# Performance work log

Hardware: AMD Instinct MI355X
Metric: run time of the kernel (lower is better)

Reference implementation:

```python
import jax, jax.numpy as jnp
import numpy as np

EMB_DIM = 1024
HEAD_DIM = 128
BLOCK_SIZE = 2048
BATCH = 8


def setup_inputs() -> dict:
    key = jax.random.key(0)
    kx, kq, kk, kv = jax.random.split(key, 4)
    x = jax.random.normal(kx, (BATCH, BLOCK_SIZE, EMB_DIM), dtype=jnp.float32)
    # nn.Linear(emb_dim, head_dim, bias=False) weights have shape [head_dim, emb_dim]
    s = 1.0 / np.sqrt(EMB_DIM)
    Wq = jax.random.uniform(kq, (HEAD_DIM, EMB_DIM), jnp.float32, -s, s)
    Wk = jax.random.uniform(kk, (HEAD_DIM, EMB_DIM), jnp.float32, -s, s)
    Wv = jax.random.uniform(kv, (HEAD_DIM, EMB_DIM), jnp.float32, -s, s)
    return {"x": x, "Wq": Wq, "Wk": Wk, "Wv": Wv}


def reference(x, Wq, Wk, Wv):
    # x: [b, t, c]; W*: [h, c]  (torch Linear applies x @ W.T)
    b, t, c = x.shape
    h = Wq.shape[0]
    q = jnp.einsum("btc,hc->bth", x, Wq)
    k = jnp.einsum("btc,hc->bth", x, Wk)
    v = jnp.einsum("btc,hc->bth", x, Wv)
    scores = jnp.einsum("bth,bsh->bts", q, k) * (h ** -0.5)  # [b, t, t]
    causal = jnp.tril(jnp.ones((t, t), dtype=bool))
    scores = jnp.where(causal, scores, -jnp.inf)
    attn = jax.nn.softmax(scores, axis=-1)
    # dropout is identity in eval / deterministic mode
    return jnp.einsum("bts,bsh->bth", attn, v)
```

## Files before the change

kernel.cpp:

```cpp
#include <hip/hip_runtime.h>
#include <hip/hip_bf16.h>

#define TT 2048
#define CC 1024
#define DD 128
#define BB 8
#define BK 32
#define NSTEP (CC / BK)

typedef __attribute__((ext_vector_type(8))) short bf16x8;
typedef __attribute__((ext_vector_type(4))) float f32x4;
typedef __attribute__((ext_vector_type(16))) float f32x16;
typedef __attribute__((ext_vector_type(4))) short short4v;

__device__ inline short f2bf(float f) {
    union { float f; unsigned u; } v; v.f = f;
    unsigned r = v.u + 0x7FFFu + ((v.u >> 16) & 1u);
    return (short)(r >> 16);
}

__device__ inline unsigned pack2(float lo, float hi) {
    return (unsigned)(unsigned short)f2bf(lo) | ((unsigned)(unsigned short)f2bf(hi) << 16);
}

#define GLOAD16(gp, lp) __builtin_amdgcn_global_load_lds(                       \
    (const __attribute__((address_space(1))) unsigned int*)(const void*)(gp),   \
    (__attribute__((address_space(3))) unsigned int*)(void*)(lp), 16, 0, 0)

__global__ __launch_bounds__(256) void prep_w(const float* __restrict__ Wq,
                                              const float* __restrict__ Wk,
                                              const float* __restrict__ Wv,
                                              short* __restrict__ Wall) {
    int row = blockIdx.x;
    const float* src = row < 128 ? Wq + (size_t)row * CC
                     : row < 256 ? Wk + (size_t)(row - 128) * CC
                                 : Wv + (size_t)(row - 256) * CC;
    short* dst = Wall + (size_t)row * CC;
    int j = threadIdx.x * 4;
    float4 f = *(const float4*)(src + j);
    short4v s = { f2bf(f.x), f2bf(f.y), f2bf(f.z), f2bf(f.w) };
    *(short4v*)(dst + j) = s;
}

__global__ __launch_bounds__(512) void qkv_onepass(const float* __restrict__ X,
                                                   const short* __restrict__ Wall,
                                                   short* __restrict__ Q,
                                                   short* __restrict__ K,
                                                   short* __restrict__ Vs) {
    __shared__ char lds[2 * 32768];
    int tid = threadIdx.x, lane = tid & 63, wid = tid >> 6;
    int wm = wid >> 2, wn = wid & 3;
    int lg = lane >> 4, lr = lane & 15;
    int m0 = blockIdx.x * 64;

    int rA = tid >> 3, cA = (tid & 7) * 16;
    int sA = cA ^ ((rA & 7) << 4);
    const char* gA = (const char*)(X + (size_t)(m0 + rA) * CC) + sA;
    int rB0 = tid >> 2, cB = (tid & 3) * 16;
    const char* gB = (const char*)Wall + cB;

    f32x4 acc[2][6] = {};

#define STAGE1(t_, buf_) do {                                                   \
        char* b_ = lds + (buf_) * 32768;                                        \
        GLOAD16(gA + (size_t)(t_) * 128, b_ + tid * 16);                        \
        _Pragma("unroll")                                                       \
        for (int i_ = 0; i_ < 3; ++i_)                                          \
            GLOAD16(gB + (size_t)(rB0 + i_ * 128) * 2048 + (size_t)(t_) * 64,   \
                    b_ + 8192 + (tid + i_ * 512) * 16);                         \
    } while (0)

#define KSTEP1(buf_) do {                                                       \
        const char* b_ = lds + (buf_) * 32768;                                  \
        bf16x8 a_[2], bb_[6];                                                   \
        int swz_ = (lr & 7) << 4;                                               \
        _Pragma("unroll")                                                       \
        for (int mi = 0; mi < 2; ++mi) {                                        \
            const char* Ap_ = b_ + (wm * 32 + mi * 16 + lr) * 128;              \
            f32x4 lo_ = *(const f32x4*)(Ap_ + ((lg * 32) ^ swz_));              \
            f32x4 hi_ = *(const f32x4*)(Ap_ + ((lg * 32 + 16) ^ swz_));         \
            bf16x8 t_;                                                          \
            t_[0] = f2bf(lo_[0]); t_[1] = f2bf(lo_[1]);                         \
            t_[2] = f2bf(lo_[2]); t_[3] = f2bf(lo_[3]);                         \
            t_[4] = f2bf(hi_[0]); t_[5] = f2bf(hi_[1]);                         \
            t_[6] = f2bf(hi_[2]); t_[7] = f2bf(hi_[3]);                         \
            a_[mi] = t_;                                                        \
        }                                                                       \
        _Pragma("unroll")                                                       \
        for (int nj = 0; nj < 6; ++nj)                                          \
            bb_[nj] = *(const bf16x8*)(b_ + 8192 + (wn*96 + nj*16 + lr) * 64 + lg*16);\
        _Pragma("unroll")                                                       \
        for (int mi = 0; mi < 2; ++mi)                                          \
            _Pragma("unroll")                                                   \
            for (int nj = 0; nj < 6; ++nj)                                      \
                acc[mi][nj] = __builtin_amdgcn_mfma_f32_16x16x32_bf16(a_[mi], bb_[nj], acc[mi][nj], 0, 0, 0);\
    } while (0)

    STAGE1(0, 0);
#pragma unroll 2
    for (int t = 0; t < NSTEP; ++t) {
        __syncthreads();
        if (t + 1 < NSTEP) STAGE1(t + 1, (t + 1) & 1);
        KSTEP1(t & 1);
    }
#undef STAGE1
#undef KSTEP1

    int bidx = m0 >> 11;
#pragma unroll
    for (int mi = 0; mi < 2; ++mi) {
        int row = m0 + wm * 32 + mi * 16 + lg * 4;
        int t = row - bidx * TT;
#pragma unroll
        for (int nj = 0; nj < 6; ++nj) {
            int col = wn * 96 + nj * 16 + lr;
            if (col < 128) {
                short* dst = Q + ((size_t)bidx * TT + t) * DD + col;
#pragma unroll
                for (int r = 0; r < 4; ++r) dst[(size_t)r * DD] = f2bf(acc[mi][nj][r]);
            } else if (col < 256) {
                short* dst = K + ((size_t)bidx * TT + t) * DD + (col - 128);
#pragma unroll
                for (int r = 0; r < 4; ++r) dst[(size_t)r * DD] = f2bf(acc[mi][nj][r]);
            } else {
                short4v v4;
#pragma unroll
                for (int r = 0; r < 4; ++r) v4[r] = f2bf(acc[mi][nj][r]);
                *(short4v*)(Vs + (size_t)bidx * TT * DD
                               + (size_t)(t >> 4) * 2048 + (col - 256) * 16 + (t & 15)) = v4;
            }
        }
    }
}

#define PV_CHUNK(WS, H, CB) do {                                                   \
    unsigned a0 = WS[4*(H)+0], a1 = WS[4*(H)+1];                                   \
    unsigned b0 = WS[4*(H)+2], b1 = WS[4*(H)+3];                                   \
    unsigned xa0 = (unsigned)__shfl_xor((int)a0, 32, 64);                          \
    unsigned xa1 = (unsigned)__shfl_xor((int)a1, 32, 64);                          \
    unsigned xb0 = (unsigned)__shfl_xor((int)b0, 32, 64);                          \
    unsigned xb1 = (unsigned)__shfl_xor((int)b1, 32, 64);                          \
    union { unsigned u[4]; bf16x8 v; } pu;                                         \
    pu.u[0] = lg2 ? xb0 : a0;                                                      \
    pu.u[1] = lg2 ? xb1 : a1;                                                      \
    pu.u[2] = lg2 ? b0  : xa0;                                                     \
    pu.u[3] = lg2 ? b1  : xa1;                                                     \
    _Pragma("unroll")                                                              \
    for (int dt = 0; dt < 4; ++dt)                                                 \
        acc[dt] = __builtin_amdgcn_mfma_f32_32x32x16_bf16(vf[CB][dt], pu.v, acc[dt], 0,0,0);\
} while (0)

__global__ __launch_bounds__(256) void attn32(const short* __restrict__ Q,
                                              const short* __restrict__ K,
                                              const short* __restrict__ Vt,
                                              float* __restrict__ out) {
    __shared__ float slot[2][4][32][33];
    __shared__ float ml[2][2][32];

    int tid = threadIdx.x;
    int lane = tid & 63, w = tid >> 6;
    int q = lane & 31, lg2 = lane >> 5;
    int bid = blockIdx.x;
    int b = bid & 7;
    int qt = 63 - (bid >> 3);
    int r0 = qt * 32;
    int qq = r0 + q;

    const short* Qb = Q + (size_t)b * TT * DD;
    const short* Kb = K + (size_t)b * TT * DD;
    const short* Vb = Vt + (size_t)b * TT * DD;

    bf16x8 qf[8];
#pragma unroll
    for (int kc = 0; kc < 8; ++kc)
        qf[kc] = *(const bf16x8*)(Qb + (size_t)qq * DD + kc * 16 + lg2 * 8);

    f32x16 acc[4] = {};
    float mb = -INFINITY, l = 0.f;
    const float scale = 0.08838834764831845f;
    int kend = r0 + 32;

    for (int kt = w; kt * 64 < kend; kt += 4) {
        int kbase = kt * 64;
        f32x16 s0 = {}, s1 = {};
        const short* Kp0 = Kb + (size_t)(kbase + q) * DD + lg2 * 8;
        const short* Kp1 = Kp0 + (size_t)32 * DD;
#pragma unroll
        for (int kc = 0; kc < 8; ++kc) {
            bf16x8 k0 = *(const bf16x8*)(Kp0 + kc * 16);
            bf16x8 k1 = *(const bf16x8*)(Kp1 + kc * 16);
            s0 = __builtin_amdgcn_mfma_f32_32x32x16_bf16(k0, qf[kc], s0, 0, 0, 0);
            s1 = __builtin_amdgcn_mfma_f32_32x32x16_bf16(k1, qf[kc], s1, 0, 0, 0);
        }

        bf16x8 vf[4][4];
#pragma unroll
        for (int cb = 0; cb < 4; ++cb) {
            const short* Vp = Vb + ((size_t)((kbase >> 4) + cb) * 128 + q) * 16 + lg2 * 8;
#pragma unroll
            for (int dt = 0; dt < 4; ++dt)
                vf[cb][dt] = *(const bf16x8*)(Vp + dt * 512);
        }

        if (kbase + 63 > r0) {
#pragma unroll
            for (int r = 0; r < 16; ++r) {
                int kl = (r & 3) + 8 * (r >> 2) + 4 * lg2;
                s0[r] = (kbase + kl > qq) ? -INFINITY : s0[r] * scale;
                s1[r] = (kbase + 32 + kl > qq) ? -INFINITY : s1[r] * scale;
            }
        } else {
#pragma unroll
            for (int r = 0; r < 16; ++r) { s0[r] *= scale; s1[r] *= scale; }
        }

        float tmx[16];
#pragma unroll
        for (int r = 0; r < 16; ++r) tmx[r] = fmaxf(s0[r], s1[r]);
#pragma unroll
        for (int st = 8; st; st >>= 1)
#pragma unroll
            for (int r = 0; r < 8; ++r) if (r < st) tmx[r] = fmaxf(tmx[r], tmx[r + st]);
        float pm = fmaxf(tmx[0], __shfl_xor(tmx[0], 32, 64));

        if (__any(pm > mb + 8.f)) {
            float mn = fmaxf(mb, pm);
            float mc = (mn == -INFINITY) ? 0.f : mn;
            float sc = __expf(mb - mc);
            mb = mc; l *= sc;
#pragma unroll
            for (int dt = 0; dt < 4; ++dt)
#pragma unroll
                for (int r = 0; r < 16; ++r) acc[dt][r] *= sc;
        }

#pragma unroll
        for (int r = 0; r < 16; ++r) { s0[r] = __expf(s0[r] - mb); s1[r] = __expf(s1[r] - mb); }

        float ts[16];
#pragma unroll
        for (int r = 0; r < 16; ++r) ts[r] = s0[r] + s1[r];
#pragma unroll
        for (int st = 8; st; st >>= 1)
#pragma unroll
            for (int r = 0; r < 8; ++r) if (r < st) ts[r] += ts[r + st];
        l += ts[0] + __shfl_xor(ts[0], 32, 64);

        unsigned w0[8], w1[8];
#pragma unroll
        for (int k2 = 0; k2 < 8; ++k2) {
            w0[k2] = pack2(s0[2 * k2], s0[2 * k2 + 1]);
            w1[k2] = pack2(s1[2 * k2], s1[2 * k2 + 1]);
        }

        PV_CHUNK(w0, 0, 0);
        PV_CHUNK(w0, 1, 1);
        PV_CHUNK(w1, 0, 2);
        PV_CHUNK(w1, 1, 3);
    }

    if (w >= 2) {
        int s = w - 2;
#pragma unroll
        for (int dt = 0; dt < 4; ++dt)
#pragma unroll
            for (int r = 0; r < 16; ++r)
                slot[s][dt][(r & 3) + 8 * (r >> 2) + 4 * lg2][q] = acc[dt][r];
        if (lg2 == 0) { ml[s][0][q] = mb; ml[s][1][q] = l; }
    }
    __syncthreads();
    if (w < 2) {
        int s = w;
        float m2 = ml[s][0][q], l2 = ml[s][1][q];
        float M = fmaxf(mb, m2);
        float Mc = (M == -INFINITY) ? 0.f : M;
        float e1 = __expf(mb - Mc), e2 = __expf(m2 - Mc);
        mb = Mc; l = l * e1 + l2 * e2;
#pragma unroll
        for (int dt = 0; dt < 4; ++dt)
#pragma unroll
            for (int r = 0; r < 16; ++r)
                acc[dt][r] = acc[dt][r] * e1 + slot[s][dt][(r & 3) + 8 * (r >> 2) + 4 * lg2][q] * e2;
    }
    __syncthreads();
    if (w == 1) {
#pragma unroll
        for (int dt = 0; dt < 4; ++dt)
#pragma unroll
            for (int r = 0; r < 16; ++r)
                slot[0][dt][(r & 3) + 8 * (r >> 2) + 4 * lg2][q] = acc[dt][r];
        if (lg2 == 0) { ml[0][0][q] = mb; ml[0][1][q] = l; }
    }
    __syncthreads();
    if (w == 0) {
        float m2 = ml[0][0][q], l2 = ml[0][1][q];
        float M = fmaxf(mb, m2);
        float Mc = (M == -INFINITY) ? 0.f : M;
        float e1 = __expf(mb - Mc), e2 = __expf(m2 - Mc);
        l = l * e1 + l2 * e2;
        float inv = 1.f / l;
#pragma unroll
        for (int dt = 0; dt < 4; ++dt)
#pragma unroll
            for (int rq = 0; rq < 4; ++rq) {
                f32x4 o4;
#pragma unroll
                for (int j = 0; j < 4; ++j) {
                    int r = rq * 4 + j;
                    o4[j] = (acc[dt][r] * e1 + slot[0][dt][(r & 3) + 8 * rq + 4 * lg2][q] * e2) * inv;
                }
                *(f32x4*)(out + ((size_t)b * TT + qq) * DD + dt * 32 + rq * 8 + lg2 * 4) = o4;
            }
    }
}

extern "C" void kernel_launch(void* const* d_in, const int* in_sizes, int n_in,
                              void* d_out, int out_size, void* d_ws, size_t ws_size,
                              hipStream_t stream) {
    const float* x  = (const float*)d_in[0];
    const float* Wq = (const float*)d_in[1];
    const float* Wk = (const float*)d_in[2];
    const float* Wv = (const float*)d_in[3];
    float* out = (float*)d_out;

    char* ws = (char*)d_ws;
    short* Wall = (short*)ws;
    short* Q    = (short*)(ws + 786432);
    short* K    = (short*)(ws + 786432 + 4194304);
    short* Vs   = (short*)(ws + 786432 + 2 * 4194304);

    prep_w<<<384, 256, 0, stream>>>(Wq, Wk, Wv, Wall);
    qkv_onepass<<<256, 512, 0, stream>>>(x, Wall, Q, K, Vs);
    attn32<<<BB * 64, 256, 0, stream>>>(Q, K, Vs, out);
}
```

Baseline: 71.26 us.

## Shrink QKV projection tile to 32 rows with 256-thread blocks and k-major W layout

The QKV projection kernel now handles 32 rows of X per block with 4 waves instead of 64 rows with 8 waves, doubling the grid to 512 blocks to fill more of the 256 CUs. The weight tile in LDS is re-laid out k-chunk-major so each MFMA B-fragment read is a contiguous 16-byte slice, which should change the bank-access pattern. In exchange, every block re-reads the full weight matrix for half as many rows, so global weight traffic doubles and the number of loads per thread per stage rises.

Measured after the change: 128.1 us. 79.8% more time.

```diff
diff --git a/kernel.cpp b/kernel.cpp
--- a/kernel.cpp
+++ b/kernel.cpp
@@ -42,41 +42,46 @@
     *(short4v*)(dst + j) = s;
 }
 
-__global__ __launch_bounds__(512) void qkv_onepass(const float* __restrict__ X,
-                                                   const short* __restrict__ Wall,
-                                                   short* __restrict__ Q,
-                                                   short* __restrict__ K,
-                                                   short* __restrict__ Vs) {
-    __shared__ char lds[2 * 32768];
-    int tid = threadIdx.x, lane = tid & 63, wid = tid >> 6;
-    int wm = wid >> 2, wn = wid & 3;
+__global__ __launch_bounds__(256) void qkv_op32(const float* __restrict__ X,
+                                                const short* __restrict__ Wall,
+                                                short* __restrict__ Q,
+                                                short* __restrict__ K,
+                                                short* __restrict__ Vs) {
+    __shared__ char lds[2 * 28672];
+    int tid = threadIdx.x, lane = tid & 63, wn = tid >> 6;
     int lg = lane >> 4, lr = lane & 15;
-    int m0 = blockIdx.x * 64;
+    int m0 = blockIdx.x * 32;
 
     int rA = tid >> 3, cA = (tid & 7) * 16;
     int sA = cA ^ ((rA & 7) << 4);
-    const char* gA = (const char*)(X + (size_t)(m0 + rA) * CC) + sA;
-    int rB0 = tid >> 2, cB = (tid & 3) * 16;
-    const char* gB = (const char*)Wall + cB;
+    const char* gA = (const char*)X + (size_t)(m0 + rA) * 4096 + sA;
+    int skc[6], snn[6];
+#pragma unroll
+    for (int i = 0; i < 6; ++i) {
+        int s = i * 256 + tid;
+        skc[i] = s / 384;
+        snn[i] = s - skc[i] * 384;
+    }
+    const char* gB = (const char*)Wall;
 
     f32x4 acc[2][6] = {};
 
-#define STAGE1(t_, buf_) do {                                                   \
-        char* b_ = lds + (buf_) * 32768;                                        \
+#define STAGE2(t_, buf_) do {                                                   \
+        char* b_ = lds + (buf_) * 28672;                                        \
         GLOAD16(gA + (size_t)(t_) * 128, b_ + tid * 16);                        \
         _Pragma("unroll")                                                       \
-        for (int i_ = 0; i_ < 3; ++i_)                                          \
-            GLOAD16(gB + (size_t)(rB0 + i_ * 128) * 2048 + (size_t)(t_) * 64,   \
-                    b_ + 8192 + (tid + i_ * 512) * 16);                         \
+        for (int i_ = 0; i_ < 6; ++i_)                                          \
+            GLOAD16(gB + (size_t)snn[i_] * 2048 + (size_t)(t_) * 64 + skc[i_] * 16,\
+                    b_ + 4096 + i_ * 4096 + tid * 16);                          \
     } while (0)
 
-#define KSTEP1(buf_) do {                                                       \
-        const char* b_ = lds + (buf_) * 32768;                                  \
+#define KSTEP2(buf_) do {                                                       \
+        const char* b_ = lds + (buf_) * 28672;                                  \
         bf16x8 a_[2], bb_[6];                                                   \
         int swz_ = (lr & 7) << 4;                                               \
         _Pragma("unroll")                                                       \
         for (int mi = 0; mi < 2; ++mi) {                                        \
-            const char* Ap_ = b_ + (wm * 32 + mi * 16 + lr) * 128;              \
+            const char* Ap_ = b_ + (mi * 16 + lr) * 128;                        \
             f32x4 lo_ = *(const f32x4*)(Ap_ + ((lg * 32) ^ swz_));              \
             f32x4 hi_ = *(const f32x4*)(Ap_ + ((lg * 32 + 16) ^ swz_));         \
             bf16x8 t_;                                                          \
@@ -88,7 +93,8 @@
         }                                                                       \
         _Pragma("unroll")                                                       \
         for (int nj = 0; nj < 6; ++nj)                                          \
-            bb_[nj] = *(const bf16x8*)(b_ + 8192 + (wn*96 + nj*16 + lr) * 64 + lg*16);\
+            bb_[nj] = *(const bf16x8*)(b_ + 4096 +                              \
+                        (lg * 384 + wn * 96 + nj * 16 + lr) * 16);              \
         _Pragma("unroll")                                                       \
         for (int mi = 0; mi < 2; ++mi)                                          \
             _Pragma("unroll")                                                   \
@@ -96,20 +102,20 @@
                 acc[mi][nj] = __builtin_amdgcn_mfma_f32_16x16x32_bf16(a_[mi], bb_[nj], acc[mi][nj], 0, 0, 0);\
     } while (0)
 
-    STAGE1(0, 0);
+    STAGE2(0, 0);
 #pragma unroll 2
     for (int t = 0; t < NSTEP; ++t) {
         __syncthreads();
-        if (t + 1 < NSTEP) STAGE1(t + 1, (t + 1) & 1);
-        KSTEP1(t & 1);
-    }
-#undef STAGE1
-#undef KSTEP1
+        if (t + 1 < NSTEP) STAGE2(t + 1, (t + 1) & 1);
+        KSTEP2(t & 1);
+    }
+#undef STAGE2
+#undef KSTEP2
 
     int bidx = m0 >> 11;
 #pragma unroll
     for (int mi = 0; mi < 2; ++mi) {
-        int row = m0 + wm * 32 + mi * 16 + lg * 4;
+        int row = m0 + mi * 16 + lg * 4;
         int t = row - bidx * TT;
 #pragma unroll
         for (int nj = 0; nj < 6; ++nj) {
@@ -330,6 +336,6 @@
     short* Vs   = (short*)(ws + 786432 + 2 * 4194304);
 
     prep_w<<<384, 256, 0, stream>>>(Wq, Wk, Wv, Wall);
-    qkv_onepass<<<256, 512, 0, stream>>>(x, Wall, Q, K, Vs);
+    qkv_op32<<<512, 256, 0, stream>>>(x, Wall, Q, K, Vs);
     attn32<<<BB * 64, 256, 0, stream>>>(Q, K, Vs, out);
 }
```
